# Optimization experiments

Measured on AMD Instinct MI355X. Metric: run time of the kernel, lower is better.

The kernel has to match this reference:

```python
import jax, jax.numpy as jnp
import numpy as np


def setup_inputs() -> dict:
    key = jax.random.key(0)
    T, TOK, D = 16, 4096, 2048
    C = D // 2          # comp_dim
    H = 2 * C           # MLP hidden = comp_dim * 2
    K = 16              # comp_len
    NN = T * (TOK // 2)  # node rows == edge rows == 32768
    ks = jax.random.split(key, 10)
    x = jax.random.normal(ks[0], (T, TOK, D), dtype=jnp.float32)
    # structured ragged layout: first half of tokens are nodes, second half edges
    padded_node_mask = jnp.zeros((T, TOK), dtype=bool).at[:, :TOK // 2].set(True)
    padded_edge_mask = jnp.logical_not(padded_node_mask)
    rand_indices = jax.random.randint(ks[1], (2 * K, 1000), 0, NN)
    s = 0.02
    node_W1 = s * jax.random.normal(ks[2], (K, D, H), dtype=jnp.float32)
    node_b1 = jnp.zeros((K, H), dtype=jnp.float32)
    node_W2 = s * jax.random.normal(ks[3], (K, H, C), dtype=jnp.float32)
    node_b2 = jnp.zeros((K, C), dtype=jnp.float32)
    edge_W1 = s * jax.random.normal(ks[4], (K, D, H), dtype=jnp.float32)
    edge_b1 = jnp.zeros((K, H), dtype=jnp.float32)
    edge_W2 = s * jax.random.normal(ks[5], (K, H, C), dtype=jnp.float32)
    edge_b2 = jnp.zeros((K, C), dtype=jnp.float32)
    return {"x": x, "padded_node_mask": padded_node_mask,
            "padded_edge_mask": padded_edge_mask, "rand_indices": rand_indices,
            "node_W1": node_W1, "node_b1": node_b1, "node_W2": node_W2, "node_b2": node_b2,
            "edge_W1": edge_W1, "edge_b1": edge_b1, "edge_W2": edge_W2, "edge_b2": edge_b2}


def _branch(rows, seg, idx, W1, b1, W2, b2, T, TOK, NROWS, C):
    # rows: [NROWS, D] gathered tokens; seg: [NROWS] timestamp id per row
    # idx:  [K, 1000] sampled rows per component MLP
    sel = rows[idx]                                                # [K,1000,D]
    h = jax.nn.gelu(jnp.einsum('kld,kdh->klh', sel, W1) + b1[:, None, :],
                    approximate=False)
    h = jnp.einsum('klh,khc->klc', h, W2) + b2[:, None, :]         # [K,1000,C]

    def step(carry, args):
        i, hh = args
        # scatter-set dedupes duplicate sampled indices (same value anyway),
        # matching torch's zeros[...] = mlp(...) assignment semantics
        z = jnp.zeros((NROWS, C), dtype=hh.dtype).at[i].set(hh)    # sparse rows
        pooled = jax.ops.segment_sum(z, seg, num_segments=T)       # [T,C]
        return carry, pooled

    _, pooled = jax.lax.scan(step, None, (idx, h))                 # [K,T,C]
    # adaptive_avg_pool1d(..., 1) == mean over the full token dim (incl. zeros)
    return pooled / TOK


def reference(x, padded_node_mask, padded_edge_mask, rand_indices,
              node_W1, node_b1, node_W2, node_b2,
              edge_W1, edge_b1, edge_W2, edge_b2):
    T, TOK, D = x.shape
    C = D // 2
    K = node_W1.shape[0]
    NN = T * TOK // 2  # node rows (== edge rows for our structured masks)
    nt, ntok = jnp.nonzero(padded_node_mask, size=NN)
    et, etok = jnp.nonzero(padded_edge_mask, size=NN)
    nodes = x[nt, ntok]  # [NN, D], row-major order like torch x[mask]
    edges = x[et, etok]
    node_pooled = _branch(nodes, nt, rand_indices[:K],
                          node_W1, node_b1, node_W2, node_b2, T, TOK, NN, C)
    edge_pooled = _branch(edges, et, rand_indices[K:],
                          edge_W1, edge_b1, edge_W2, edge_b2, T, TOK, NN, C)
    comp = jnp.concatenate([node_pooled, edge_pooled], axis=0)     # [2K,T,C]
    # cat along feature dim in component order -> [T, 1, 2K*C]
    compressed_x = comp.transpose(1, 0, 2).reshape(T, 1, 2 * K * C)
    return compressed_x
```

## Files before the change

kernel.cpp:

```cpp
#include <hip/hip_runtime.h>
#include <math.h>


typedef __attribute__((ext_vector_type(8))) short bf16x8;
typedef __attribute__((ext_vector_type(4))) short s16x4;
typedef __attribute__((ext_vector_type(4))) float f32x4;
typedef unsigned int u32;

constexpr int TT    = 16;
constexpr int TOKN  = 4096;
constexpr int DD    = 2048;
constexpr int HH    = 2048;
constexpr int CC    = 1024;
constexpr int LL    = 1000;
constexpr int NCOMP = 32;
constexpr int MP    = 1024;
constexpr int BMX = 256, BNX = 128;
constexpr int MTX  = MP / BMX;
constexpr int NT1 = HH / BNX;
constexpr int NT2 = CC / BNX;
constexpr int NT  = 2048 / 64;

__device__ __forceinline__ short f2bf(float f) {
  __bf16 h = (__bf16)f;
  return *reinterpret_cast<short*>(&h);
}
__device__ __forceinline__ int swz(int row) {
  return (row & 7) ^ ((row >> 3) & 7);
}
__device__ __forceinline__ int sw(int row, int gran) {
  return (row << 6) + ((gran ^ swz(row)) << 3);
}
__device__ __forceinline__ void gl_lds16(const void* g, void* l) {
  __builtin_amdgcn_global_load_lds(
      (const __attribute__((address_space(1))) u32*)g,
      (__attribute__((address_space(3))) u32*)l, 16, 0, 0);
}

__global__ void dedup_kernel(const int* __restrict__ ridx,
                             unsigned* __restrict__ bitmap,
                             float* __restrict__ keepf) {
  int comp = blockIdx.x;
  for (int l = threadIdx.x; l < MP; l += 256) {
    float kv = 0.0f;
    if (l < LL) {
      int r = ridx[comp * LL + l];
      unsigned bit = 1u << (r & 31);
      unsigned old = atomicOr(&bitmap[(comp << 10) + (r >> 5)], bit);
      kv = (old & bit) ? 0.0f : 1.0f;
    }
    keepf[(comp << 10) + l] = kv;
  }
}

__global__ __launch_bounds__(256) void gather_kernel(
    const float* __restrict__ x, const int* __restrict__ ridx,
    short* __restrict__ Ab) {
  int bid = blockIdx.x;
  int comp = bid >> 7, rgrp = bid & 127;
  int t = threadIdx.x;
  int tr = t >> 5, tn = t & 31;
  int m = rgrp * 8 + tr;
  int mi = m < LL ? m : LL - 1;
  int r = ridx[comp * LL + mi];
  int tokoff = comp >= 16 ? TOKN / 2 : 0;
  const float* src = x + ((size_t)(r >> 11) * TOKN + (r & 2047) + tokoff) * DD;
  short* drow = Ab + ((size_t)(comp * MP + m)) * DD;
  int s_m = swz(m);
#pragma unroll
  for (int i = 0; i < 8; ++i) {
    int gi = tn + 32 * i;
    float4 f0 = *reinterpret_cast<const float4*>(src + gi * 8);
    float4 f1 = *reinterpret_cast<const float4*>(src + gi * 8 + 4);
    bf16x8 pk;
    pk[0]=f2bf(f0.x); pk[1]=f2bf(f0.y); pk[2]=f2bf(f0.z); pk[3]=f2bf(f0.w);
    pk[4]=f2bf(f1.x); pk[5]=f2bf(f1.y); pk[6]=f2bf(f1.z); pk[7]=f2bf(f1.w);
    int c = gi >> 3, g = gi & 7;
    *reinterpret_cast<bf16x8*>(&drow[c * 64 + ((g ^ s_m) << 3)]) = pk;
  }
}

template<int LDW>
__device__ __forceinline__ void kloop(
    const short* __restrict__ aBase,
    const float* __restrict__ wBase,
    short* sm, f32x4 (&acc)[8][4],
    int wm, int wn, int lr, int lg, int tid) {
  const short* aSrc0 = aBase + (size_t)(tid >> 3) * 2048 + (tid & 7) * 8;
  int ldsA0 = tid * 8;
  int tn = tid & 31, tkb = tid >> 5, bn0 = tn * 4;
  const float* wCol = wBase + bn0;

  float4 brB[8];

  auto aglds = [&](int t, int buf) {
    short* l = sm + buf * 16384;
#pragma unroll
    for (int q = 0; q < 8; ++q)
      gl_lds16(aSrc0 + (size_t)q * 65536 + t * 64, l + ldsA0 + q * 2048);
  };
  auto bload = [&](int t) {
    const float* bb = wCol + (size_t)(t * 64 + tkb * 8) * LDW;
#pragma unroll
    for (int i = 0; i < 8; ++i)
      brB[i] = *reinterpret_cast<const float4*>(bb + (size_t)i * LDW);
  };
  auto bwrite = [&]() {
    short* Bs = sm + 32768;
#pragma unroll
    for (int j = 0; j < 4; ++j) {
      bf16x8 pk;
#pragma unroll
      for (int i = 0; i < 8; ++i) pk[i] = f2bf((&brB[i].x)[j]);
      *reinterpret_cast<bf16x8*>(&Bs[sw(bn0 + j, tkb)]) = pk;
    }
  };
  auto compute = [&](int d) {
    const short* A = sm + d * 16384;
    const short* B = sm + 32768;
#pragma unroll
    for (int kk = 0; kk < 2; ++kk) {
      bf16x8 af[8], bfr[4];
#pragma unroll
      for (int i = 0; i < 8; ++i)
        af[i] = *reinterpret_cast<const bf16x8*>(&A[sw(wm + i * 16 + lr, kk * 4 + lg)]);
#pragma unroll
      for (int j = 0; j < 4; ++j)
        bfr[j] = *reinterpret_cast<const bf16x8*>(&B[sw(wn + j * 16 + lr, kk * 4 + lg)]);
      __builtin_amdgcn_s_setprio(1);
#pragma unroll
      for (int i = 0; i < 8; ++i)
#pragma unroll
        for (int j = 0; j < 4; ++j)
          acc[i][j] = __builtin_amdgcn_mfma_f32_16x16x32_bf16(af[i], bfr[j], acc[i][j], 0, 0, 0);
      __builtin_amdgcn_s_setprio(0);
    }
  };

  bload(0);
  aglds(0, 0);
  bwrite();
  bload(1);
  aglds(1, 1);
  asm volatile("s_waitcnt lgkmcnt(0)" ::: "memory");
  __builtin_amdgcn_s_barrier();

#pragma unroll 1
  for (int t = 0; t < NT; ++t) {
    if (t < NT - 1) {
      asm volatile("s_waitcnt vmcnt(16)" ::: "memory");
    } else {
      asm volatile("s_waitcnt vmcnt(0)" ::: "memory");
    }
    __builtin_amdgcn_sched_barrier(0);
    compute(t & 1);
    __builtin_amdgcn_s_barrier();
    if (t + 1 < NT) {
      bwrite();
      if (t + 2 < NT) {
        bload(t + 2);
        aglds(t + 2, t & 1);
      }
      asm volatile("s_waitcnt lgkmcnt(0)" ::: "memory");
      __builtin_amdgcn_s_barrier();
    }
  }
}

__global__ __launch_bounds__(256, 2) void gemm1_kernel(
    const float* __restrict__ nW1, const float* __restrict__ nb1,
    const float* __restrict__ eW1, const float* __restrict__ eb1,
    const short* __restrict__ Ab, short* __restrict__ hbuf) {
  __shared__ short smem[40960];

  constexpr int NWG = NCOMP * MTX * NT1;
  constexpr int CPX = NWG / 8;
  int b0 = blockIdx.x;
  int lb = (b0 & 7) * CPX + (b0 >> 3);
  int comp = lb / (MTX * NT1);
  int rem  = lb % (MTX * NT1);
  int mt = rem / NT1, nt = rem % NT1;
  bool isEdge = comp >= 16;
  int k16 = isEdge ? comp - 16 : comp;
  const float* W1 = (isEdge ? eW1 : nW1) + (size_t)k16 * DD * HH;
  const float* b1 = (isEdge ? eb1 : nb1) + (size_t)k16 * HH;

  int tid = threadIdx.x, lane = tid & 63, wid = tid >> 6;
  int wm = (wid >> 1) << 7, wn = (wid & 1) << 6;
  int lr = lane & 15, lg = lane >> 4;

  f32x4 acc[8][4] = {};
  kloop<HH>(Ab + ((size_t)(comp * MP + mt * BMX)) * DD,
            W1 + nt * BNX, smem, acc, wm, wn, lr, lg, tid);

  __builtin_amdgcn_s_barrier();
  short* Cs = smem;
  const float* b1p = b1 + nt * BNX;
#pragma unroll
  for (int i = 0; i < 8; ++i)
#pragma unroll
    for (int j = 0; j < 4; ++j) {
      int nl = wn + j * 16 + lr;
      float bias = b1p[nl];
#pragma unroll
      for (int rr = 0; rr < 4; ++rr) {
        int ml = wm + i * 16 + lg * 4 + rr;
        float v = acc[i][j][rr] + bias;
        float ge = 0.5f * v * (1.0f + erff(v * 0.70710678118654752f));
        Cs[ml * 132 + nl] = f2bf(ge);
      }
    }
  __syncthreads();
  short* hrow = hbuf + ((size_t)(comp * MP + mt * BMX)) * HH;
#pragma unroll
  for (int q = 0; q < 32; ++q) {
    int gl = q * 256 + tid;
    int r = gl >> 5, gg = gl & 31;
    s16x4 v = *reinterpret_cast<const s16x4*>(&Cs[r * 132 + gg * 4]);
    int dst = (nt * 2 + (gg >> 4)) * 64 + ((((gg >> 1) & 7) ^ swz(r)) << 3) + (gg & 1) * 4;
    *reinterpret_cast<s16x4*>(&hrow[(size_t)r * HH + dst]) = v;
  }
}

__global__ __launch_bounds__(256, 2) void gemm2_kernel(
    const short* __restrict__ hbuf, const int* __restrict__ ridx,
    const float* __restrict__ nW2, const float* __restrict__ nb2,
    const float* __restrict__ eW2, const float* __restrict__ eb2,
    const float* __restrict__ keepf, float* __restrict__ partial) {
  __shared__ short smem[40960];

  constexpr int NWG = NCOMP * MTX * NT2;
  constexpr int CPX = NWG / 8;
  int b0 = blockIdx.x;
  int lb = (b0 & 7) * CPX + (b0 >> 3);
  int comp = lb / (MTX * NT2);
  int rem  = lb % (MTX * NT2);
  int mt = rem / NT2, nt = rem % NT2;
  bool isEdge = comp >= 16;
  int k16 = isEdge ? comp - 16 : comp;
  const float* W2 = (isEdge ? eW2 : nW2) + (size_t)k16 * HH * CC;
  const float* b2 = (isEdge ? eb2 : nb2) + (size_t)k16 * CC;

  int tid = threadIdx.x, lane = tid & 63, wid = tid >> 6;
  int wm = (wid >> 1) << 7, wn = (wid & 1) << 6;
  int lr = lane & 15, lg = lane >> 4;

  f32x4 acc[8][4] = {};
  kloop<CC>(hbuf + ((size_t)(comp * MP + mt * BMX)) * HH,
            W2 + nt * BNX, smem, acc, wm, wn, lr, lg, tid);

  __builtin_amdgcn_s_barrier();
  float* part = (float*)smem;
  int*   tarr = (int*)((char*)smem + 16640);
  float* karr = (float*)((char*)smem + 17664);
  if (tid < BMX) {
    int mglob = mt * BMX + tid;
    int mi = mglob < LL ? mglob : LL - 1;
    int r2 = ridx[comp * LL + mi];
    tarr[tid] = r2 >> 11;
    karr[tid] = keepf[(comp << 10) + mglob];
  }
  for (int e = tid; e < TT * 257; e += 256) part[e] = 0.0f;
  __syncthreads();
  const float* b2p = b2 + nt * BNX;
#pragma unroll
  for (int i = 0; i < 8; ++i)
#pragma unroll
    for (int j = 0; j < 4; ++j) {
      int nl = wn + j * 16 + lr;
      float bias = b2p[nl];
#pragma unroll
      for (int rr = 0; rr < 4; ++rr) {
        int ml = wm + i * 16 + lg * 4 + rr;
        float v = (acc[i][j][rr] + bias) * karr[ml];
        atomicAdd(&part[tarr[ml] * 257 + nl], v);
      }
    }
  __syncthreads();
  float* pout = partial + ((size_t)(comp * MTX + mt)) * TT * CC + nt * BNX;
  for (int e = tid; e < TT * BNX; e += 256) {
    int t2 = e >> 7, c = e & 127;
    pout[(size_t)t2 * CC + c] = part[t2 * 257 + c];
  }
}

__global__ void reduce_kernel(const float* __restrict__ partial,
                              float* __restrict__ out) {
  int idx = blockIdx.x * 256 + threadIdx.x;
  int c    = idx & (CC - 1);
  int comp = (idx >> 10) & (NCOMP - 1);
  int t    = idx >> 15;
  float s = 0.0f;
#pragma unroll
  for (int mt = 0; mt < MTX; ++mt)
    s += partial[(((size_t)(comp * MTX + mt)) * TT + t) * CC + c];
  out[idx] = s * (1.0f / 4096.0f);
}

extern "C" void kernel_launch(void* const* d_in, const int* in_sizes, int n_in,
                              void* d_out, int out_size, void* d_ws, size_t ws_size,
                              hipStream_t stream) {
  const float* x    = (const float*)d_in[0];
  const int*   ridx = (const int*)d_in[3];
  const float* nW1  = (const float*)d_in[4];
  const float* nb1  = (const float*)d_in[5];
  const float* nW2  = (const float*)d_in[6];
  const float* nb2  = (const float*)d_in[7];
  const float* eW1  = (const float*)d_in[8];
  const float* eb1  = (const float*)d_in[9];
  const float* eW2  = (const float*)d_in[10];
  const float* eb2  = (const float*)d_in[11];
  float* out = (float*)d_out;

  const size_t H_B   = (size_t)NCOMP * MP * HH * 2;
  const size_t BMP_B = (size_t)NCOMP * 1024 * 4;
  const size_t KP_B  = (size_t)NCOMP * 1024 * 4;
  const size_t PRT_B = (size_t)NCOMP * MTX * TT * CC * 4;
  const size_t base  = H_B + BMP_B + KP_B + PRT_B;

  char* ws = (char*)d_ws;
  short* hbuf      = (short*)ws;
  unsigned* bitmap = (unsigned*)(ws + H_B);
  float* keepf     = (float*)(ws + H_B + BMP_B);
  float* partial   = (float*)(ws + H_B + BMP_B + KP_B);
  short* Ab        = (short*)(ws + base);

  hipMemsetAsync(bitmap, 0, BMP_B, stream);
  dedup_kernel<<<NCOMP, 256, 0, stream>>>(ridx, bitmap, keepf);
  gather_kernel<<<NCOMP * 128, 256, 0, stream>>>(x, ridx, Ab);
  gemm1_kernel<<<NCOMP * MTX * NT1, 256, 0, stream>>>(nW1, nb1, eW1, eb1, Ab, hbuf);
  gemm2_kernel<<<NCOMP * MTX * NT2, 256, 0, stream>>>(hbuf, ridx, nW2, nb2, eW2, eb2, keepf, partial);
  reduce_kernel<<<out_size / 256, 256, 0, stream>>>(partial, out);
}
```

Measured before the change: 806.3 us.

## Pool GELU activations before second GEMM using linearity of segment sum

```diff
diff --git a/kernel.cpp b/kernel.cpp
--- a/kernel.cpp
+++ b/kernel.cpp
@@ -3,7 +3,6 @@
 
 
 typedef __attribute__((ext_vector_type(8))) short bf16x8;
-typedef __attribute__((ext_vector_type(4))) short s16x4;
 typedef __attribute__((ext_vector_type(4))) float f32x4;
 typedef unsigned int u32;
 
@@ -18,8 +17,7 @@
 constexpr int BMX = 256, BNX = 128;
 constexpr int MTX  = MP / BMX;
 constexpr int NT1 = HH / BNX;
-constexpr int NT2 = CC / BNX;
-constexpr int NT  = 2048 / 64;
+constexpr int NT  = DD / 64;
 
 __device__ __forceinline__ short f2bf(float f) {
   __bf16 h = (__bf16)f;
@@ -39,18 +37,24 @@
 
 __global__ void dedup_kernel(const int* __restrict__ ridx,
                              unsigned* __restrict__ bitmap,
-                             float* __restrict__ keepf) {
+                             float* __restrict__ keepf,
+                             int* __restrict__ counts) {
+  __shared__ int cnt[TT];
   int comp = blockIdx.x;
+  if (threadIdx.x < TT) cnt[threadIdx.x] = 0;
+  __syncthreads();
   for (int l = threadIdx.x; l < MP; l += 256) {
     float kv = 0.0f;
     if (l < LL) {
       int r = ridx[comp * LL + l];
       unsigned bit = 1u << (r & 31);
       unsigned old = atomicOr(&bitmap[(comp << 10) + (r >> 5)], bit);
-      kv = (old & bit) ? 0.0f : 1.0f;
+      if (!(old & bit)) { kv = 1.0f; atomicAdd(&cnt[r >> 11], 1); }
     }
     keepf[(comp << 10) + l] = kv;
   }
+  __syncthreads();
+  if (threadIdx.x < TT) counts[comp * TT + threadIdx.x] = cnt[threadIdx.x];
 }
 
 __global__ __launch_bounds__(256) void gather_kernel(
@@ -170,7 +174,8 @@
 __global__ __launch_bounds__(256, 2) void gemm1_kernel(
     const float* __restrict__ nW1, const float* __restrict__ nb1,
     const float* __restrict__ eW1, const float* __restrict__ eb1,
-    const short* __restrict__ Ab, short* __restrict__ hbuf) {
+    const short* __restrict__ Ab, const int* __restrict__ ridx,
+    const float* __restrict__ keepf, float* __restrict__ partial) {
   __shared__ short smem[40960];
 
   constexpr int NWG = NCOMP * MTX * NT1;
@@ -194,66 +199,10 @@
             W1 + nt * BNX, smem, acc, wm, wn, lr, lg, tid);
 
   __builtin_amdgcn_s_barrier();
-  short* Cs = smem;
-  const float* b1p = b1 + nt * BNX;
-#pragma unroll
-  for (int i = 0; i < 8; ++i)
-#pragma unroll
-    for (int j = 0; j < 4; ++j) {
-      int nl = wn + j * 16 + lr;
-      float bias = b1p[nl];
-#pragma unroll
-      for (int rr = 0; rr < 4; ++rr) {
-        int ml = wm + i * 16 + lg * 4 + rr;
-        float v = acc[i][j][rr] + bias;
-        float ge = 0.5f * v * (1.0f + erff(v * 0.70710678118654752f));
-        Cs[ml * 132 + nl] = f2bf(ge);
-      }
-    }
-  __syncthreads();
-  short* hrow = hbuf + ((size_t)(comp * MP + mt * BMX)) * HH;
-#pragma unroll
-  for (int q = 0; q < 32; ++q) {
-    int gl = q * 256 + tid;
-    int r = gl >> 5, gg = gl & 31;
-    s16x4 v = *reinterpret_cast<const s16x4*>(&Cs[r * 132 + gg * 4]);
-    int dst = (nt * 2 + (gg >> 4)) * 64 + ((((gg >> 1) & 7) ^ swz(r)) << 3) + (gg & 1) * 4;
-    *reinterpret_cast<s16x4*>(&hrow[(size_t)r * HH + dst]) = v;
-  }
-}
-
-__global__ __launch_bounds__(256, 2) void gemm2_kernel(
-    const short* __restrict__ hbuf, const int* __restrict__ ridx,
-    const float* __restrict__ nW2, const float* __restrict__ nb2,
-    const float* __restrict__ eW2, const float* __restrict__ eb2,
-    const float* __restrict__ keepf, float* __restrict__ partial) {
-  __shared__ short smem[40960];
-
-  constexpr int NWG = NCOMP * MTX * NT2;
-  constexpr int CPX = NWG / 8;
-  int b0 = blockIdx.x;
-  int lb = (b0 & 7) * CPX + (b0 >> 3);
-  int comp = lb / (MTX * NT2);
-  int rem  = lb % (MTX * NT2);
-  int mt = rem / NT2, nt = rem % NT2;
-  bool isEdge = comp >= 16;
-  int k16 = isEdge ? comp - 16 : comp;
-  const float* W2 = (isEdge ? eW2 : nW2) + (size_t)k16 * HH * CC;
-  const float* b2 = (isEdge ? eb2 : nb2) + (size_t)k16 * CC;
-
-  int tid = threadIdx.x, lane = tid & 63, wid = tid >> 6;
-  int wm = (wid >> 1) << 7, wn = (wid & 1) << 6;
-  int lr = lane & 15, lg = lane >> 4;
-
-  f32x4 acc[8][4] = {};
-  kloop<CC>(hbuf + ((size_t)(comp * MP + mt * BMX)) * HH,
-            W2 + nt * BNX, smem, acc, wm, wn, lr, lg, tid);
-
-  __builtin_amdgcn_s_barrier();
   float* part = (float*)smem;
-  int*   tarr = (int*)((char*)smem + 16640);
-  float* karr = (float*)((char*)smem + 17664);
-  if (tid < BMX) {
+  int*   tarr = (int*)((char*)smem + 16448);
+  float* karr = (float*)((char*)smem + 17472);
+  {
     int mglob = mt * BMX + tid;
     int mi = mglob < LL ? mglob : LL - 1;
     int r2 = ridx[comp * LL + mi];
@@ -262,39 +211,73 @@
   }
   for (int e = tid; e < TT * 257; e += 256) part[e] = 0.0f;
   __syncthreads();
-  const float* b2p = b2 + nt * BNX;
+  const float* b1p = b1 + nt * BNX;
 #pragma unroll
   for (int i = 0; i < 8; ++i)
 #pragma unroll
     for (int j = 0; j < 4; ++j) {
       int nl = wn + j * 16 + lr;
-      float bias = b2p[nl];
+      float bias = b1p[nl];
 #pragma unroll
       for (int rr = 0; rr < 4; ++rr) {
         int ml = wm + i * 16 + lg * 4 + rr;
-        float v = (acc[i][j][rr] + bias) * karr[ml];
-        atomicAdd(&part[tarr[ml] * 257 + nl], v);
+        float v = acc[i][j][rr] + bias;
+        float ge = 0.5f * v * (1.0f + erff(v * 0.70710678118654752f));
+        atomicAdd(&part[tarr[ml] * 257 + nl], ge * karr[ml]);
       }
     }
   __syncthreads();
-  float* pout = partial + ((size_t)(comp * MTX + mt)) * TT * CC + nt * BNX;
+  float* pout = partial + ((size_t)(comp * MTX + mt) * TT) * HH + nt * BNX;
   for (int e = tid; e < TT * BNX; e += 256) {
     int t2 = e >> 7, c = e & 127;
-    pout[(size_t)t2 * CC + c] = part[t2 * 257 + c];
-  }
-}
-
-__global__ void reduce_kernel(const float* __restrict__ partial,
-                              float* __restrict__ out) {
-  int idx = blockIdx.x * 256 + threadIdx.x;
-  int c    = idx & (CC - 1);
-  int comp = (idx >> 10) & (NCOMP - 1);
-  int t    = idx >> 15;
-  float s = 0.0f;
-#pragma unroll
-  for (int mt = 0; mt < MTX; ++mt)
-    s += partial[(((size_t)(comp * MTX + mt)) * TT + t) * CC + c];
-  out[idx] = s * (1.0f / 4096.0f);
+    pout[(size_t)t2 * HH + c] = part[t2 * 257 + c];
+  }
+}
+
+__global__ __launch_bounds__(256) void gemm3_kernel(
+    const float* __restrict__ partial, const int* __restrict__ counts,
+    const float* __restrict__ nW2, const float* __restrict__ nb2,
+    const float* __restrict__ eW2, const float* __restrict__ eb2,
+    float* __restrict__ out) {
+  __shared__ float hs[TT * 256];
+  int bid = blockIdx.x;
+  int comp = bid >> 3, chunk = bid & 7;
+  bool isEdge = comp >= 16;
+  int k16 = isEdge ? comp - 16 : comp;
+  const float* W2 = (isEdge ? eW2 : nW2) + (size_t)k16 * HH * CC;
+  const float* b2 = (isEdge ? eb2 : nb2) + (size_t)k16 * CC;
+  int tid = threadIdx.x;
+  int col = chunk * 128 + (tid & 127);
+  int tg = tid >> 7;
+  float acc[8] = {};
+  const float* pbase = partial + (size_t)comp * MTX * TT * HH;
+
+  for (int kb = 0; kb < HH / 256; ++kb) {
+    __syncthreads();
+    for (int q = 0; q < 16; ++q) {
+      int idx = q * 256 + tid;
+      int t = idx >> 8, k = idx & 255;
+      float s = 0.0f;
+#pragma unroll
+      for (int mt = 0; mt < MTX; ++mt)
+        s += pbase[((size_t)(mt * TT + t)) * HH + kb * 256 + k];
+      hs[t * 256 + k] = s;
+    }
+    __syncthreads();
+#pragma unroll 4
+    for (int k = 0; k < 256; ++k) {
+      float w = W2[(size_t)(kb * 256 + k) * CC + col];
+#pragma unroll
+      for (int tt = 0; tt < 8; ++tt)
+        acc[tt] += hs[(tg * 8 + tt) * 256 + k] * w;
+    }
+  }
+#pragma unroll
+  for (int tt = 0; tt < 8; ++tt) {
+    int t = tg * 8 + tt;
+    float v = (acc[tt] + (float)counts[comp * TT + t] * b2[col]) * (1.0f / 4096.0f);
+    out[(size_t)t * 32768 + comp * 1024 + col] = v;
+  }
 }
 
 extern "C" void kernel_launch(void* const* d_in, const int* in_sizes, int n_in,
@@ -312,23 +295,21 @@
   const float* eb2  = (const float*)d_in[11];
   float* out = (float*)d_out;
 
-  const size_t H_B   = (size_t)NCOMP * MP * HH * 2;
   const size_t BMP_B = (size_t)NCOMP * 1024 * 4;
   const size_t KP_B  = (size_t)NCOMP * 1024 * 4;
-  const size_t PRT_B = (size_t)NCOMP * MTX * TT * CC * 4;
-  const size_t base  = H_B + BMP_B + KP_B + PRT_B;
+  const size_t CNT_B = (size_t)NCOMP * TT * 4;
+  const size_t PRT_B = (size_t)NCOMP * MTX * TT * HH * 4;
 
   char* ws = (char*)d_ws;
-  short* hbuf      = (short*)ws;
-  unsigned* bitmap = (unsigned*)(ws + H_B);
-  float* keepf     = (float*)(ws + H_B + BMP_B);
-  float* partial   = (float*)(ws + H_B + BMP_B + KP_B);
-  short* Ab        = (short*)(ws + base);
+  unsigned* bitmap = (unsigned*)ws;
+  float* keepf     = (float*)(ws + BMP_B);
+  int* counts      = (int*)(ws + BMP_B + KP_B);
+  float* partial   = (float*)(ws + BMP_B + KP_B + CNT_B);
+  short* Ab        = (short*)(ws + BMP_B + KP_B + CNT_B + PRT_B);
 
   hipMemsetAsync(bitmap, 0, BMP_B, stream);
-  dedup_kernel<<<NCOMP, 256, 0, stream>>>(ridx, bitmap, keepf);
+  dedup_kernel<<<NCOMP, 256, 0, stream>>>(ridx, bitmap, keepf, counts);
   gather_kernel<<<NCOMP * 128, 256, 0, stream>>>(x, ridx, Ab);
-  gemm1_kernel<<<NCOMP * MTX * NT1, 256, 0, stream>>>(nW1, nb1, eW1, eb1, Ab, hbuf);
-  gemm2_kernel<<<NCOMP * MTX * NT2, 256, 0, stream>>>(hbuf, ridx, nW2, nb2, eW2, eb2, keepf, partial);
-  reduce_kernel<<<out_size / 256, 256, 0, stream>>>(partial, out);
-}
+  gemm1_kernel<<<NCOMP * MTX * NT1, 256, 0, stream>>>(nW1, nb1, eW1, eb1, Ab, ridx, keepf, partial);
+  gemm3_kernel<<<NCOMP * 8, 256, 0, stream>>>(partial, counts, nW2, nb2, eW2, eb2, out);
+}
```

Measured after the change: 990.0 us. 22.8% more time.
